# Kernel optimization log

Hardware: AMD Instinct MI355X
Metric: run time of the kernel (lower is better)

The kernel has to match this reference:

```python
import jax, jax.numpy as jnp
import numpy as np

N, E, D = 50000, 600000, 128  # nodes, edges, units (== vert_dim, so no W_adapt)


def glorot(key, shape):
    lim = np.sqrt(6.0 / (shape[0] + shape[1]))
    return jax.random.uniform(key, shape, jnp.float32, -lim, lim)


def setup_inputs() -> dict:
    key = jax.random.key(0)
    ks = jax.random.split(key, 8)
    X = jax.random.normal(ks[0], (N, D), jnp.float32)
    ref_a = jax.random.randint(ks[1], (E,), 0, N, jnp.int32)
    ref_b = jax.random.randint(ks[2], (E,), 0, N, jnp.int32)
    # msg_net: two Dense(D) layers, inner_activation=None (linear)
    W1 = glorot(ks[3], (D, D)); b1 = jnp.zeros((D,), jnp.float32)
    W2 = glorot(ks[4], (D, D)); b2 = jnp.zeros((D,), jnp.float32)
    # keras GRUCell (reset_after=True): kernel [D,3D], recurrent_kernel [D,3D], bias [2,3D]
    gru_kernel = glorot(ks[5], (D, 3 * D))
    gru_rkernel = glorot(ks[6], (D, 3 * D))
    gru_bias = jnp.zeros((2, 3 * D), jnp.float32)
    return {"X": X, "ref_a": ref_a, "ref_b": ref_b,
            "W1": W1, "b1": b1, "W2": W2, "b2": b2,
            "gru_kernel": gru_kernel, "gru_rkernel": gru_rkernel, "gru_bias": gru_bias}


def _ggnn(X, ref_a, ref_b, W1, b1, W2, b2, gru_kernel, gru_rkernel, gru_bias):
    # msg_net (depth=2, linear inner activation)
    X_msg = (X @ W1 + b1) @ W2 + b2                       # [N, D]
    # wl1_convolution, undirected: scatter-add both directions
    agg = jnp.zeros_like(X_msg)
    agg = agg.at[ref_b].add(X_msg[ref_a])                 # a -> b
    agg = agg.at[ref_a].add(X_msg[ref_b])                 # b -> a (directed=False)
    # keras GRUCell update: inputs = agg, state = X  (reset_after=True)
    mx = agg @ gru_kernel + gru_bias[0]                   # [N, 3D]
    mh = X @ gru_rkernel + gru_bias[1]                    # [N, 3D]
    xz, xr, xh = jnp.split(mx, 3, axis=-1)
    rz, rr, rh = jnp.split(mh, 3, axis=-1)
    z = jax.nn.sigmoid(xz + rz)
    r = jax.nn.sigmoid(xr + rr)
    hh = jnp.tanh(xh + r * rh)
    return z * X + (1.0 - z) * hh                         # [N, D]


def reference(X, ref_a, ref_b, W1, b1, W2, b2, gru_kernel, gru_rkernel, gru_bias):
    return _ggnn(X, ref_a, ref_b, W1, b1, W2, b2, gru_kernel, gru_rkernel, gru_bias)
```

## Files before the change

### kernel.cpp

```cpp
#include <hip/hip_runtime.h>
#include <cstdint>
#include <cstddef>

typedef __bf16 bf16x8 __attribute__((ext_vector_type(8)));
typedef float  f32x4  __attribute__((ext_vector_type(4)));
typedef short  s16x8  __attribute__((ext_vector_type(8)));

static __device__ __forceinline__ float bf2f(short s) {
    union { unsigned u; float f; } v;
    v.u = ((unsigned)(unsigned short)s) << 16;
    return v.f;
}
static __device__ __forceinline__ short f2bf(float f) {
    unsigned u = __float_as_uint(f);
    u += 0x7fffu + ((u >> 16) & 1u);
    return (short)(u >> 16);
}
static __device__ __forceinline__ float sigmoid_(float x) {
    return 1.0f / (1.0f + __expf(-x));
}
static __device__ __forceinline__ float tanh_(float x) {
    float ax = fabsf(x);
    float e  = __expf(-2.0f * ax);
    float t  = (1.0f - e) / (1.0f + e);
    return copysignf(t, x);
}

#define MFMA(a, b, c) __builtin_amdgcn_mfma_f32_16x16x32_bf16((a), (b), (c), 0, 0, 0)

static __device__ __forceinline__ int lidx8(int r, int ch) {
    return r * 128 + ((ch ^ (r & 15)) << 3);
}
static __device__ __forceinline__ int lidx(int r, int col) {
    return r * 128 + ((((col >> 3) ^ (r & 15)) << 3) | (col & 7));
}

#define BLOCKS1     256
#define STRIPE_CAP  64
#define BUCKET_REG  (BLOCKS1 * STRIPE_CAP)
#define NODE_CAP    96
#define SENTINEL    0xFFFFFFFFu

static __device__ __forceinline__ s16x8 cvt8(const float* p) {
    f32x4 a0 = *(const f32x4*)(p);
    f32x4 a1 = *(const f32x4*)(p + 4);
    s16x8 v;
    v[0] = f2bf(a0[0]); v[1] = f2bf(a0[1]); v[2] = f2bf(a0[2]); v[3] = f2bf(a0[3]);
    v[4] = f2bf(a1[0]); v[5] = f2bf(a1[1]); v[6] = f2bf(a1[2]); v[7] = f2bf(a1[3]);
    return v;
}

__global__ __launch_bounds__(256) void prep_kernel(
    const int* __restrict__ ra, const int* __restrict__ rb,
    unsigned* __restrict__ bucketed, int E, int CPB, int nbuckets,
    const float* __restrict__ W1, const float* __restrict__ W2,
    const float* __restrict__ GK, const float* __restrict__ GR,
    short* __restrict__ W1t, short* __restrict__ W2t,
    short* __restrict__ GKt, short* __restrict__ GRt)
{
    __shared__ int cnt[256];
    cnt[threadIdx.x] = 0;

    int i = blockIdx.x * 256 + threadIdx.x;
    if (i < 16384) {
        int k = i >> 7, n = i & 127;
        W1t[n * 128 + k] = f2bf(W1[i]);
        W2t[n * 128 + k] = f2bf(W2[i]);
    }
    if (i < 49152) {
        int k = i / 384, n = i - k * 384;
        GKt[n * 128 + k] = f2bf(GK[i]);
        GRt[n * 128 + k] = f2bf(GR[i]);
    }
    __syncthreads();

    const int blk = blockIdx.x;
    const int e1 = min(E, (blk + 1) * CPB);
    for (int e = blk * CPB + threadIdx.x; e < e1; e += 256) {
        int a = ra[e], b = rb[e];
        int ka = a >> 8, kb = b >> 8;
        int r1 = atomicAdd(&cnt[ka], 1);
        if (r1 < STRIPE_CAP)
            bucketed[(size_t)ka * BUCKET_REG + blk * STRIPE_CAP + r1] =
                ((unsigned)(a & 255) << 16) | (unsigned)b;
        int r2 = atomicAdd(&cnt[kb], 1);
        if (r2 < STRIPE_CAP)
            bucketed[(size_t)kb * BUCKET_REG + blk * STRIPE_CAP + r2] =
                ((unsigned)(b & 255) << 16) | (unsigned)a;
    }
    __syncthreads();
    const int total = nbuckets * STRIPE_CAP;
    for (int j = threadIdx.x; j < total; j += 256) {
        int k = j >> 6, slot = j & (STRIPE_CAP - 1);
        if (slot >= min(cnt[k], STRIPE_CAP))
            bucketed[(size_t)k * BUCKET_REG + blk * STRIPE_CAP + slot] = SENTINEL;
    }
}

__global__ __launch_bounds__(512) void msg_pass2_kernel(
    const float* __restrict__ X, const short* __restrict__ W1t,
    const float* __restrict__ b1, const short* __restrict__ W2t,
    const float* __restrict__ b2, short* __restrict__ msg, int N, int nblk64,
    const unsigned* __restrict__ bucketed, unsigned short* __restrict__ nbrS,
    int* __restrict__ counts)
{
    __shared__ short ldsA[64 * 128];
    __shared__ short ldsY[64 * 128];
    __shared__ int off[256];
    const int tid = threadIdx.x;

    if ((int)blockIdx.x >= nblk64) {
        const int k = blockIdx.x - nblk64;
        if (tid < 256) off[tid] = 0;
        __syncthreads();
        const int lo = k << 8;
        const unsigned* reg = bucketed + (size_t)k * BUCKET_REG;
        for (int i = tid; i < BUCKET_REG; i += 512) {
            unsigned e = reg[i];
            if (e != SENTINEL) {
                int nl = (int)(e >> 16);
                int p  = (int)(e & 0xffffu);
                int r  = atomicAdd(&off[nl], 1);
                if (r < NODE_CAP)
                    nbrS[(size_t)(lo + nl) * NODE_CAP + r] = (unsigned short)p;
            }
        }
        __syncthreads();
        int node = lo + tid;
        if (tid < 256 && node < N) counts[node] = min(off[tid], NODE_CAP);
        return;
    }

    const int m0   = blockIdx.x * 64;
    const int lane = tid & 63, wv = tid >> 6;
    const int q = lane >> 4, c = lane & 15;
    const int ncol = wv * 16 + c;

    bf16x8 w1f[4], w2f[4];
#pragma unroll
    for (int ks = 0; ks < 4; ks++) {
        int ko = ks * 32 + q * 8;
        w1f[ks] = __builtin_bit_cast(bf16x8, *(const s16x8*)(W1t + (size_t)ncol * 128 + ko));
        w2f[ks] = __builtin_bit_cast(bf16x8, *(const s16x8*)(W2t + (size_t)ncol * 128 + ko));
    }

    for (int i = tid; i < 64 * 16; i += 512) {
        int r = i >> 4, ch = i & 15;
        s16x8 v;
        if (m0 + r < N) v = cvt8(X + (size_t)(m0 + r) * 128 + ch * 8);
        else            v = (s16x8)0;
        *(s16x8*)(ldsA + lidx8(r, ch)) = v;
    }
    __syncthreads();

    f32x4 acc[4];
#pragma unroll
    for (int rt = 0; rt < 4; rt++) acc[rt] = (f32x4)0.0f;
#pragma unroll
    for (int ks = 0; ks < 4; ks++) {
        int kc = ks * 4 + q;
#pragma unroll
        for (int rt = 0; rt < 4; rt++) {
            bf16x8 aA = __builtin_bit_cast(bf16x8, *(const s16x8*)(ldsA + lidx8(rt * 16 + c, kc)));
            acc[rt] = MFMA(aA, w1f[ks], acc[rt]);
        }
    }
    float bias1 = b1[ncol];
#pragma unroll
    for (int rt = 0; rt < 4; rt++)
#pragma unroll
        for (int i = 0; i < 4; i++)
            ldsY[lidx(rt * 16 + q * 4 + i, ncol)] = f2bf(acc[rt][i] + bias1);
    __syncthreads();

#pragma unroll
    for (int rt = 0; rt < 4; rt++) acc[rt] = (f32x4)0.0f;
#pragma unroll
    for (int ks = 0; ks < 4; ks++) {
        int kc = ks * 4 + q;
#pragma unroll
        for (int rt = 0; rt < 4; rt++) {
            bf16x8 aY = __builtin_bit_cast(bf16x8, *(const s16x8*)(ldsY + lidx8(rt * 16 + c, kc)));
            acc[rt] = MFMA(aY, w2f[ks], acc[rt]);
        }
    }
    float bias2 = b2[ncol];
#pragma unroll
    for (int rt = 0; rt < 4; rt++)
#pragma unroll
        for (int i = 0; i < 4; i++) {
            int row = m0 + rt * 16 + q * 4 + i;
            if (row < N) msg[(size_t)row * 128 + ncol] = f2bf(acc[rt][i] + bias2);
        }
}

__global__ __launch_bounds__(256) void gather_kernel(
    const short* __restrict__ msg, const unsigned short* __restrict__ nbrS,
    const int* __restrict__ counts, short* __restrict__ aggb, int N)
{
    const int lane = threadIdx.x & 63;
    const int node = blockIdx.x * 4 + (threadIdx.x >> 6);
    if (node >= N) return;
    const int g  = lane >> 4;
    const int cl = lane & 15;
    const int s   = node * NODE_CAP;
    const int end = s + counts[node];

    float a[8];
#pragma unroll
    for (int t = 0; t < 8; t++) a[t] = 0.0f;

    int i = s + g;
    for (; i + 12 < end; i += 16) {
        int j0 = (int)nbrS[i];
        int j1 = (int)nbrS[i + 4];
        int j2 = (int)nbrS[i + 8];
        int j3 = (int)nbrS[i + 12];
        s16x8 p0 = *(const s16x8*)(msg + (size_t)j0 * 128 + cl * 8);
        s16x8 p1 = *(const s16x8*)(msg + (size_t)j1 * 128 + cl * 8);
        s16x8 p2 = *(const s16x8*)(msg + (size_t)j2 * 128 + cl * 8);
        s16x8 p3 = *(const s16x8*)(msg + (size_t)j3 * 128 + cl * 8);
#pragma unroll
        for (int t = 0; t < 8; t++) a[t] += bf2f(p0[t]);
#pragma unroll
        for (int t = 0; t < 8; t++) a[t] += bf2f(p1[t]);
#pragma unroll
        for (int t = 0; t < 8; t++) a[t] += bf2f(p2[t]);
#pragma unroll
        for (int t = 0; t < 8; t++) a[t] += bf2f(p3[t]);
    }
    for (; i < end; i += 4) {
        int j = (int)nbrS[i];
        s16x8 p = *(const s16x8*)(msg + (size_t)j * 128 + cl * 8);
#pragma unroll
        for (int t = 0; t < 8; t++) a[t] += bf2f(p[t]);
    }

#pragma unroll
    for (int t = 0; t < 8; t++) {
        a[t] += __shfl_xor(a[t], 32);
        a[t] += __shfl_xor(a[t], 16);
    }
    if (g == 0) {
        s16x8 o;
#pragma unroll
        for (int t = 0; t < 8; t++) o[t] = f2bf(a[t]);
        *(s16x8*)(aggb + (size_t)node * 128 + cl * 8) = o;
    }
}

__global__ __launch_bounds__(512) void gru_kernel(
    const short* __restrict__ aggb, const float* __restrict__ X,
    const short* __restrict__ GKt, const short* __restrict__ GRt,
    const float* __restrict__ gbias, float* __restrict__ out, int N)
{
    __shared__ short ldsA[64 * 128];
    __shared__ short ldsX[64 * 128];
    const int tid  = threadIdx.x;
    const int m0   = blockIdx.x * 64;
    const int lane = tid & 63, wv = tid >> 6;
    const int q = lane >> 4, c = lane & 15;
    const int ncol = wv * 16 + c;

    bf16x8 bkz[4], bkr[4], bkh[4], brz[4], brr[4], brh[4];
#pragma unroll
    for (int ks = 0; ks < 4; ks++) {
        int ko = ks * 32 + q * 8;
        bkz[ks] = __builtin_bit_cast(bf16x8, *(const s16x8*)(GKt + (size_t)(ncol)       * 128 + ko));
        bkr[ks] = __builtin_bit_cast(bf16x8, *(const s16x8*)(GKt + (size_t)(128 + ncol) * 128 + ko));
        bkh[ks] = __builtin_bit_cast(bf16x8, *(const s16x8*)(GKt + (size_t)(256 + ncol) * 128 + ko));
        brz[ks] = __builtin_bit_cast(bf16x8, *(const s16x8*)(GRt + (size_t)(ncol)       * 128 + ko));
        brr[ks] = __builtin_bit_cast(bf16x8, *(const s16x8*)(GRt + (size_t)(128 + ncol) * 128 + ko));
        brh[ks] = __builtin_bit_cast(bf16x8, *(const s16x8*)(GRt + (size_t)(256 + ncol) * 128 + ko));
    }
    float bz0 = gbias[ncol],       br0 = gbias[128 + ncol],       bh0 = gbias[256 + ncol];
    float bz1 = gbias[384 + ncol], br1 = gbias[384 + 128 + ncol], bh1 = gbias[384 + 256 + ncol];

    for (int i = tid; i < 64 * 16; i += 512) {
        int r = i >> 4, ch = i & 15;
        s16x8 vx, va;
        if (m0 + r < N) {
            vx = cvt8(X + (size_t)(m0 + r) * 128 + ch * 8);
            va = *(const s16x8*)(aggb + (size_t)(m0 + r) * 128 + ch * 8);
        } else { vx = (s16x8)0; va = (s16x8)0; }
        *(s16x8*)(ldsX + lidx8(r, ch)) = vx;
        *(s16x8*)(ldsA + lidx8(r, ch)) = va;
    }
    __syncthreads();

#pragma clang loop unroll(disable)
    for (int rt = 0; rt < 4; rt++) {
        float xv[4];
#pragma unroll
        for (int i = 0; i < 4; i++) {
            int grow = m0 + rt * 16 + q * 4 + i;
            xv[i] = (grow < N) ? X[(size_t)grow * 128 + ncol] : 0.0f;
        }
        f32x4 axz = (f32x4)0.0f, axr = (f32x4)0.0f, axh = (f32x4)0.0f;
        f32x4 arz = (f32x4)0.0f, arr = (f32x4)0.0f, arh = (f32x4)0.0f;
#pragma unroll
        for (int ks = 0; ks < 4; ks++) {
            int kc = ks * 4 + q;
            bf16x8 aA = __builtin_bit_cast(bf16x8, *(const s16x8*)(ldsA + lidx8(rt * 16 + c, kc)));
            bf16x8 aX = __builtin_bit_cast(bf16x8, *(const s16x8*)(ldsX + lidx8(rt * 16 + c, kc)));
            axz = MFMA(aA, bkz[ks], axz);
            axr = MFMA(aA, bkr[ks], axr);
            axh = MFMA(aA, bkh[ks], axh);
            arz = MFMA(aX, brz[ks], arz);
            arr = MFMA(aX, brr[ks], arr);
            arh = MFMA(aX, brh[ks], arh);
        }
#pragma unroll
        for (int i = 0; i < 4; i++) {
            int grow = m0 + rt * 16 + q * 4 + i;
            if (grow < N) {
                float z  = sigmoid_(axz[i] + bz0 + arz[i] + bz1);
                float r  = sigmoid_(axr[i] + br0 + arr[i] + br1);
                float hh = tanh_(axh[i] + bh0 + r * (arh[i] + bh1));
                out[(size_t)grow * 128 + ncol] = z * xv[i] + (1.0f - z) * hh;
            }
        }
    }
}

extern "C" void kernel_launch(void* const* d_in, const int* in_sizes, int n_in,
                              void* d_out, int out_size, void* d_ws, size_t ws_size,
                              hipStream_t stream)
{
    const float* X  = (const float*)d_in[0];
    const int*   ra = (const int*)d_in[1];
    const int*   rb = (const int*)d_in[2];
    const float* W1 = (const float*)d_in[3];
    const float* b1 = (const float*)d_in[4];
    const float* W2 = (const float*)d_in[5];
    const float* b2 = (const float*)d_in[6];
    const float* GK = (const float*)d_in[7];
    const float* GR = (const float*)d_in[8];
    const float* GB = (const float*)d_in[9];
    const int N = in_sizes[0] / 128;
    const int E = in_sizes[1];
    float* out = (float*)d_out;

    const int nbuckets = (N + 255) >> 8;

    char* ws = (char*)d_ws;
    size_t off = 0;
    short* aggb   = (short*)(ws + off);   off += (size_t)N * 128 * 2;
    short* msg    = (short*)(ws + off);   off += (size_t)N * 128 * 2;
    short* W1t    = (short*)(ws + off);   off += 16384u * 2;
    short* W2t    = (short*)(ws + off);   off += 16384u * 2;
    short* GKt    = (short*)(ws + off);   off += 49152u * 2;
    short* GRt    = (short*)(ws + off);   off += 49152u * 2;
    unsigned* bucketed = (unsigned*)(ws + off);
    off += (size_t)nbuckets * BUCKET_REG * 4;
    unsigned short* nbrS = (unsigned short*)(ws + off);
    off += (size_t)nbuckets * 256 * NODE_CAP * 2;
    int* counts   = (int*)(ws + off);     off += (size_t)N * 4;

    const int CPB = (E + BLOCKS1 - 1) / BLOCKS1;
    prep_kernel<<<BLOCKS1, 256, 0, stream>>>(ra, rb, bucketed, E, CPB, nbuckets,
                                             W1, W2, GK, GR, W1t, W2t, GKt, GRt);

    const int nblk64 = (N + 63) / 64;
    msg_pass2_kernel<<<nblk64 + nbuckets, 512, 0, stream>>>(
        X, W1t, b1, W2t, b2, msg, N, nblk64, bucketed, nbrS, counts);

    gather_kernel<<<(N + 3) / 4, 256, 0, stream>>>(msg, nbrS, counts, aggb, N);
    gru_kernel<<<nblk64, 512, 0, stream>>>(aggb, X, GKt, GRt, GB, out, N);
}
```

Baseline: 203.6 us.

## Fuse neighbor gather into GRU kernel, writing aggregates directly to LDS

Merges the gather kernel into the GRU kernel. Each 512-thread block gathers neighbor messages for its 64 nodes straight into shared memory, then runs the GRU MFMAs. This removes the aggb round trip through global memory and one kernel launch. In exchange, parallelism drops from about 12.5k blocks of 4 nodes to about 782 blocks, each wave walks 8 nodes one after another, and the gather's latency can no longer overlap with GRU compute across kernels.

```diff
diff --git a/kernel.cpp b/kernel.cpp
--- a/kernel.cpp
+++ b/kernel.cpp
@@ -194,63 +194,9 @@
         }
 }
 
-__global__ __launch_bounds__(256) void gather_kernel(
+__global__ __launch_bounds__(512) void gather_gru_kernel(
     const short* __restrict__ msg, const unsigned short* __restrict__ nbrS,
-    const int* __restrict__ counts, short* __restrict__ aggb, int N)
-{
-    const int lane = threadIdx.x & 63;
-    const int node = blockIdx.x * 4 + (threadIdx.x >> 6);
-    if (node >= N) return;
-    const int g  = lane >> 4;
-    const int cl = lane & 15;
-    const int s   = node * NODE_CAP;
-    const int end = s + counts[node];
-
-    float a[8];
-#pragma unroll
-    for (int t = 0; t < 8; t++) a[t] = 0.0f;
-
-    int i = s + g;
-    for (; i + 12 < end; i += 16) {
-        int j0 = (int)nbrS[i];
-        int j1 = (int)nbrS[i + 4];
-        int j2 = (int)nbrS[i + 8];
-        int j3 = (int)nbrS[i + 12];
-        s16x8 p0 = *(const s16x8*)(msg + (size_t)j0 * 128 + cl * 8);
-        s16x8 p1 = *(const s16x8*)(msg + (size_t)j1 * 128 + cl * 8);
-        s16x8 p2 = *(const s16x8*)(msg + (size_t)j2 * 128 + cl * 8);
-        s16x8 p3 = *(const s16x8*)(msg + (size_t)j3 * 128 + cl * 8);
-#pragma unroll
-        for (int t = 0; t < 8; t++) a[t] += bf2f(p0[t]);
-#pragma unroll
-        for (int t = 0; t < 8; t++) a[t] += bf2f(p1[t]);
-#pragma unroll
-        for (int t = 0; t < 8; t++) a[t] += bf2f(p2[t]);
-#pragma unroll
-        for (int t = 0; t < 8; t++) a[t] += bf2f(p3[t]);
-    }
-    for (; i < end; i += 4) {
-        int j = (int)nbrS[i];
-        s16x8 p = *(const s16x8*)(msg + (size_t)j * 128 + cl * 8);
-#pragma unroll
-        for (int t = 0; t < 8; t++) a[t] += bf2f(p[t]);
-    }
-
-#pragma unroll
-    for (int t = 0; t < 8; t++) {
-        a[t] += __shfl_xor(a[t], 32);
-        a[t] += __shfl_xor(a[t], 16);
-    }
-    if (g == 0) {
-        s16x8 o;
-#pragma unroll
-        for (int t = 0; t < 8; t++) o[t] = f2bf(a[t]);
-        *(s16x8*)(aggb + (size_t)node * 128 + cl * 8) = o;
-    }
-}
-
-__global__ __launch_bounds__(512) void gru_kernel(
-    const short* __restrict__ aggb, const float* __restrict__ X,
+    const int* __restrict__ counts, const float* __restrict__ X,
     const short* __restrict__ GKt, const short* __restrict__ GRt,
     const float* __restrict__ gbias, float* __restrict__ out, int N)
 {
@@ -262,6 +208,66 @@
     const int q = lane >> 4, c = lane & 15;
     const int ncol = wv * 16 + c;
 
+    for (int i = tid; i < 64 * 16; i += 512) {
+        int r = i >> 4, ch = i & 15;
+        s16x8 vx;
+        if (m0 + r < N) vx = cvt8(X + (size_t)(m0 + r) * 128 + ch * 8);
+        else            vx = (s16x8)0;
+        *(s16x8*)(ldsX + lidx8(r, ch)) = vx;
+    }
+
+    const int g  = lane >> 4;
+    const int cl = lane & 15;
+#pragma clang loop unroll(disable)
+    for (int rr = 0; rr < 8; rr++) {
+        const int lrow = wv * 8 + rr;
+        const int node = m0 + lrow;
+        float a[8];
+#pragma unroll
+        for (int t = 0; t < 8; t++) a[t] = 0.0f;
+        if (node < N) {
+            const int s   = node * NODE_CAP;
+            const int end = s + counts[node];
+            int i = s + g;
+            for (; i + 12 < end; i += 16) {
+                int j0 = (int)nbrS[i];
+                int j1 = (int)nbrS[i + 4];
+                int j2 = (int)nbrS[i + 8];
+                int j3 = (int)nbrS[i + 12];
+                s16x8 p0 = *(const s16x8*)(msg + (size_t)j0 * 128 + cl * 8);
+                s16x8 p1 = *(const s16x8*)(msg + (size_t)j1 * 128 + cl * 8);
+                s16x8 p2 = *(const s16x8*)(msg + (size_t)j2 * 128 + cl * 8);
+                s16x8 p3 = *(const s16x8*)(msg + (size_t)j3 * 128 + cl * 8);
+#pragma unroll
+                for (int t = 0; t < 8; t++) a[t] += bf2f(p0[t]);
+#pragma unroll
+                for (int t = 0; t < 8; t++) a[t] += bf2f(p1[t]);
+#pragma unroll
+                for (int t = 0; t < 8; t++) a[t] += bf2f(p2[t]);
+#pragma unroll
+                for (int t = 0; t < 8; t++) a[t] += bf2f(p3[t]);
+            }
+            for (; i < end; i += 4) {
+                int j = (int)nbrS[i];
+                s16x8 p = *(const s16x8*)(msg + (size_t)j * 128 + cl * 8);
+#pragma unroll
+                for (int t = 0; t < 8; t++) a[t] += bf2f(p[t]);
+            }
+        }
+#pragma unroll
+        for (int t = 0; t < 8; t++) {
+            a[t] += __shfl_xor(a[t], 32);
+            a[t] += __shfl_xor(a[t], 16);
+        }
+        if (g == 0) {
+            s16x8 o;
+#pragma unroll
+            for (int t = 0; t < 8; t++) o[t] = f2bf(a[t]);
+            *(s16x8*)(ldsA + lidx8(lrow, cl)) = o;
+        }
+    }
+    __syncthreads();
+
     bf16x8 bkz[4], bkr[4], bkh[4], brz[4], brr[4], brh[4];
 #pragma unroll
     for (int ks = 0; ks < 4; ks++) {
@@ -275,18 +281,6 @@
     }
     float bz0 = gbias[ncol],       br0 = gbias[128 + ncol],       bh0 = gbias[256 + ncol];
     float bz1 = gbias[384 + ncol], br1 = gbias[384 + 128 + ncol], bh1 = gbias[384 + 256 + ncol];
-
-    for (int i = tid; i < 64 * 16; i += 512) {
-        int r = i >> 4, ch = i & 15;
-        s16x8 vx, va;
-        if (m0 + r < N) {
-            vx = cvt8(X + (size_t)(m0 + r) * 128 + ch * 8);
-            va = *(const s16x8*)(aggb + (size_t)(m0 + r) * 128 + ch * 8);
-        } else { vx = (s16x8)0; va = (s16x8)0; }
-        *(s16x8*)(ldsX + lidx8(r, ch)) = vx;
-        *(s16x8*)(ldsA + lidx8(r, ch)) = va;
-    }
-    __syncthreads();
 
 #pragma clang loop unroll(disable)
     for (int rt = 0; rt < 4; rt++) {
@@ -345,7 +339,6 @@
 
     char* ws = (char*)d_ws;
     size_t off = 0;
-    short* aggb   = (short*)(ws + off);   off += (size_t)N * 128 * 2;
     short* msg    = (short*)(ws + off);   off += (size_t)N * 128 * 2;
     short* W1t    = (short*)(ws + off);   off += 16384u * 2;
     short* W2t    = (short*)(ws + off);   off += 16384u * 2;
@@ -365,6 +358,6 @@
     msg_pass2_kernel<<<nblk64 + nbuckets, 512, 0, stream>>>(
         X, W1t, b1, W2t, b2, msg, N, nblk64, bucketed, nbrS, counts);
 
-    gather_kernel<<<(N + 3) / 4, 256, 0, stream>>>(msg, nbrS, counts, aggb, N);
-    gru_kernel<<<nblk64, 512, 0, stream>>>(aggb, X, GKt, GRt, GB, out, N);
-}
+    gather_gru_kernel<<<nblk64, 512, 0, stream>>>(
+        msg, nbrS, counts, X, GKt, GRt, GB, out, N);
+}
```

After: 252.0 us. +23.8%, slower.
